# Optimization experiments

Hardware: AMD Instinct MI355X
Metric: run time of the kernel (lower is better)

Reference implementation:

```python
import jax, jax.numpy as jnp
import numpy as np

S, B, H = 2048, 4, 2048
NH = 16
HD = H // NH


def setup_inputs() -> dict:
    key = jax.random.key(0)
    ks = jax.random.split(key, 12)
    sc = 0.02
    return {
        "x": jax.random.normal(ks[0], (S, B, H), dtype=jnp.float32),
        "ln1_g": jnp.ones((H,), jnp.float32),
        "ln1_b": jnp.zeros((H,), jnp.float32),
        "qkv_w": jax.random.normal(ks[1], (3 * H, H), jnp.float32) * sc,
        "qkv_b": jnp.zeros((3 * H,), jnp.float32),
        "proj_w": jax.random.normal(ks[2], (H, H), jnp.float32) * sc,
        "proj_b": jnp.zeros((H,), jnp.float32),
        "ln2_g": jnp.ones((H,), jnp.float32),
        "ln2_b": jnp.zeros((H,), jnp.float32),
        "fc1_w": jax.random.normal(ks[3], (4 * H, H), jnp.float32) * sc,
        "fc1_b": jnp.zeros((4 * H,), jnp.float32),
        "fc2_w": jax.random.normal(ks[4], (H, 4 * H), jnp.float32) * sc,
        "fc2_b": jnp.zeros((H,), jnp.float32),
    }


def _layernorm(x, g, b, eps=1e-5):
    mu = jnp.mean(x, axis=-1, keepdims=True)
    var = jnp.mean((x - mu) ** 2, axis=-1, keepdims=True)
    return (x - mu) * jax.lax.rsqrt(var + eps) * g + b


def reference(x, ln1_g, ln1_b, qkv_w, qkv_b, proj_w, proj_b,
              ln2_g, ln2_b, fc1_w, fc1_b, fc2_w, fc2_b):
    # x: [S, B, H] (seq-first, as in original). Dropout is identity (eval mode).
    residual = x
    h = _layernorm(x, ln1_g, ln1_b)
    qkv = h @ qkv_w.T + qkv_b                       # [S, B, 3H]
    qkv = qkv.reshape(S, B, 3, NH, HD)
    q = jnp.transpose(qkv[:, :, 0], (1, 2, 0, 3))   # [B, NH, S, HD]
    k = jnp.transpose(qkv[:, :, 1], (1, 2, 0, 3))
    v = jnp.transpose(qkv[:, :, 2], (1, 2, 0, 3))
    scores = jnp.einsum("bhsd,bhtd->bhst", q, k) / jnp.sqrt(jnp.float32(HD))
    causal = jnp.tril(jnp.ones((S, S), dtype=bool))
    scores = jnp.where(causal, scores, jnp.float32(-jnp.inf))
    attn = jax.nn.softmax(scores, axis=-1)
    out = jnp.einsum("bhst,bhtd->bhsd", attn, v)    # [B, NH, S, HD]
    out = jnp.transpose(out, (2, 0, 1, 3)).reshape(S, B, H)
    out = out @ proj_w.T + proj_b
    x = residual + out
    residual = x
    h = _layernorm(x, ln2_g, ln2_b)
    h = h @ fc1_w.T + fc1_b
    h = jax.nn.gelu(h, approximate=False)
    h = h @ fc2_w.T + fc2_b
    return residual + h
```

## Files before the change

kernel.cpp:

```cpp
#include <hip/hip_runtime.h>
#include <hip/hip_bf16.h>
#include <cstdint>
#include <cstddef>

#define TOK 8192
#define HDIM 2048
#define H3 6144

typedef float f32x4 __attribute__((ext_vector_type(4)));
typedef short bf16x8 __attribute__((ext_vector_type(8)));
typedef int   i32x4 __attribute__((ext_vector_type(4)));
typedef unsigned short u16;
typedef unsigned int u32;
typedef u32 u32x2 __attribute__((ext_vector_type(2)));
typedef u32 u32x4 __attribute__((ext_vector_type(4)));

#define SLN  28.222222f
#define SW   1058.3333f
#define DQ   3.3480095e-5f

__device__ __forceinline__ u16 f2bf(float f) {
  union { float f; u32 u; } v; v.f = f;
  u32 u = v.u;
  return (u16)((u + 0x7fffu + ((u >> 16) & 1u)) >> 16);
}

__device__ __forceinline__ int q8(float v, float s) {
  int q = (int)rintf(v * s);
  return q < -127 ? -127 : (q > 127 ? 127 : q);
}

__device__ __forceinline__ float gelu_fast(float v) {
  const float u = 0.7978845608028654f * (v + 0.044715f * v * v * v);
  const float t = 1.0f - 2.0f / (__expf(2.0f * u) + 1.0f);
  return 0.5f * v * (1.0f + t);
}

__device__ __forceinline__ void gload16(const void* g, void* l) {
  __builtin_amdgcn_global_load_lds((const __attribute__((address_space(1))) u32*)g,
                                   (__attribute__((address_space(3))) u32*)l, 16, 0, 0);
}

#define GBAR()   __builtin_amdgcn_s_barrier()
#define GLGK0()  asm volatile("s_waitcnt lgkmcnt(0)" ::: "memory")
#define GVM(n)   asm volatile("s_waitcnt vmcnt(" #n ")" ::: "memory")
#define SCHED0() __builtin_amdgcn_sched_barrier(0)

__global__ __launch_bounds__(256)
void cvt_kernel(const float* __restrict__ in, u16* __restrict__ out, int n4) {
  int i = blockIdx.x * 256 + threadIdx.x;
  if (i >= n4) return;
  float4 v = ((const float4*)in)[i];
  union { u16 o[4]; u32x2 d; } t;
  t.o[0] = f2bf(v.x); t.o[1] = f2bf(v.y); t.o[2] = f2bf(v.z); t.o[3] = f2bf(v.w);
  ((u32x2*)out)[i] = t.d;
}

__global__ __launch_bounds__(256)
void cvt_i8_kernel(const float* __restrict__ in, char* __restrict__ out, int n4) {
  int i = blockIdx.x * 256 + threadIdx.x;
  if (i >= n4) return;
  float4 v = ((const float4*)in)[i];
  union { char c[4]; u32 d; } t;
  t.c[0] = (char)q8(v.x, SW); t.c[1] = (char)q8(v.y, SW);
  t.c[2] = (char)q8(v.z, SW); t.c[3] = (char)q8(v.w, SW);
  ((u32*)out)[i] = t.d;
}

template <int I8>
__global__ __launch_bounds__(256)
void ln_kernel(const float* __restrict__ x, const float* __restrict__ g,
               const float* __restrict__ bta, u16* __restrict__ out) {
  const int row = blockIdx.x, tid = threadIdx.x;
  const int lane = tid & 63, w = tid >> 6;
  const float* xr = x + (size_t)row * HDIM + tid * 8;
  float4 a = *(const float4*)xr;
  float4 c = *(const float4*)(xr + 4);
  float s = a.x + a.y + a.z + a.w + c.x + c.y + c.z + c.w;
  float q = a.x*a.x + a.y*a.y + a.z*a.z + a.w*a.w + c.x*c.x + c.y*c.y + c.z*c.z + c.w*c.w;
#pragma unroll
  for (int m = 32; m >= 1; m >>= 1) { s += __shfl_xor(s, m, 64); q += __shfl_xor(q, m, 64); }
  __shared__ float red[8];
  if (lane == 0) { red[w] = s; red[4 + w] = q; }
  __syncthreads();
  s = red[0] + red[1] + red[2] + red[3];
  q = red[4] + red[5] + red[6] + red[7];
  const float mu = s * (1.0f / HDIM);
  const float rstd = rsqrtf(q * (1.0f / HDIM) - mu * mu + 1e-5f);
  const float* gp = g + tid * 8; const float* bp = bta + tid * 8;
  float4 g0 = *(const float4*)gp, g1 = *(const float4*)(gp + 4);
  float4 b0 = *(const float4*)bp, b1 = *(const float4*)(bp + 4);
  float v[8];
  v[0] = (a.x - mu) * rstd * g0.x + b0.x;
  v[1] = (a.y - mu) * rstd * g0.y + b0.y;
  v[2] = (a.z - mu) * rstd * g0.z + b0.z;
  v[3] = (a.w - mu) * rstd * g0.w + b0.w;
  v[4] = (c.x - mu) * rstd * g1.x + b1.x;
  v[5] = (c.y - mu) * rstd * g1.y + b1.y;
  v[6] = (c.z - mu) * rstd * g1.z + b1.z;
  v[7] = (c.w - mu) * rstd * g1.w + b1.w;
  if constexpr (I8) {
    union { char c8[8]; u32x2 d; } t;
#pragma unroll
    for (int j = 0; j < 8; ++j) t.c8[j] = (char)q8(v[j], SLN);
    *(u32x2*)((char*)out + (size_t)row * HDIM + tid * 8) = t.d;
  } else {
    union { u16 o[8]; u32x4 d; } t;
#pragma unroll
    for (int j = 0; j < 8; ++j) t.o[j] = f2bf(v[j]);
    *(u32x4*)(out + (size_t)row * HDIM + tid * 8) = t.d;
  }
}

template <int EPI, int XSWZ>
__global__ __launch_bounds__(512, 1)
void gemm256(const u16* __restrict__ A, const u16* __restrict__ Bm,
             const float* __restrict__ bias, const float* __restrict__ resid,
             u16* __restrict__ Cb, float* __restrict__ Cf, int M, int N, int K) {
  __shared__ u16 lds[65536];
  char* Lb = (char*)lds;
  const int tid = threadIdx.x;
  const int lane = tid & 63, w = tid >> 6;
  const int wm = w >> 2, wn = w & 3;
  const int l15 = lane & 15, hi = lane >> 4;

  int tm, tn;
  if constexpr (XSWZ) {
    const int gx = gridDim.x;
    const int nwg = gx * gridDim.y;
    int wgid = blockIdx.y * gx + blockIdx.x;
    wgid = (wgid & 7) * (nwg >> 3) + (wgid >> 3);
    tm = (wgid / gx) * 256; tn = (wgid % gx) * 256;
  } else {
    tm = blockIdx.y * 256; tn = blockIdx.x * 256;
  }

  const size_t rsK = (size_t)K * 2;
  const int srow8 = tid >> 3;
  const int scb   = ((tid & 7) ^ ((tid >> 3) & 7)) * 16;
  const char* gA = (const char*)A + (size_t)(tm + srow8) * rsK + scb;
  const char* gB = (const char*)Bm + (size_t)(tn + srow8) * rsK + scb;

#define STGH(o, h, tt) do {                                                    \
    char* _d = Lb + ((((tt) & 1) << 16) + (o) * 32768 + (h) * 16384 + tid * 16); \
    const char* _s = (o) ? gB : gA;                                            \
    const size_t _off = (size_t)(tt) * 128 + (size_t)((h) * 128) * rsK;        \
    gload16(_s + _off, _d);                                                    \
    gload16(_s + _off + (size_t)64 * rsK, _d + 8192);                          \
  } while (0)

  int koff[2];
#pragma unroll
  for (int ks = 0; ks < 2; ++ks) koff[ks] = ((ks * 4 + hi) ^ (l15 & 7)) * 16;

#define LDA(qm, dst) do {                                                      \
    _Pragma("unroll")                                                          \
    for (int mi4 = 0; mi4 < 4; ++mi4)                                          \
      _Pragma("unroll")                                                        \
      for (int ks = 0; ks < 2; ++ks)                                           \
        dst[mi4][ks] = *(const bf16x8*)(Lb + bb + wm * 16384 +                 \
            ((qm) * 64 + mi4 * 16 + l15) * 128 + koff[ks]);                    \
  } while (0)

#define LDB(qn) do {                                                           \
    _Pragma("unroll")                                                          \
    for (int ni = 0; ni < 2; ++ni)                                             \
      _Pragma("unroll")                                                        \
      for (int ks = 0; ks < 2; ++ks)                                           \
        bf[ni][ks] = *(const bf16x8*)(Lb + bb + 32768 + (wn >> 1) * 16384 +    \
            ((wn & 1) * 64 + (qn) * 32 + ni * 16 + l15) * 128 + koff[ks]);     \
  } while (0)

#define MFMA16(qm, qn, src) do {                                               \
    __builtin_amdgcn_s_setprio(1);                                             \
    _Pragma("unroll")                                                          \
    for (int ks = 0; ks < 2; ++ks)                                             \
      _Pragma("unroll")                                                        \
      for (int mi4 = 0; mi4 < 4; ++mi4)                                        \
        _Pragma("unroll")                                                      \
        for (int ni = 0; ni < 2; ++ni)                                         \
          acc[(qm) * 4 + mi4][(qn) * 2 + ni] =                                 \
            __builtin_amdgcn_mfma_f32_16x16x32_bf16(src[mi4][ks], bf[ni][ks],  \
                acc[(qm) * 4 + mi4][(qn) * 2 + ni], 0, 0, 0);                  \
    __builtin_amdgcn_s_setprio(0);                                             \
  } while (0)

  f32x4 acc[8][4] = {};
  bf16x8 af0[4][2], af1[4][2], bf[2][2];

  const int NT = K >> 6;

  STGH(0, 0, 0); STGH(0, 1, 0); STGH(1, 0, 0); STGH(1, 1, 0);
  STGH(0, 0, 1); STGH(0, 1, 1);
  SCHED0(); GVM(4); GBAR();

  for (int t = 0; t < NT; ++t) {
    const int bb = (t & 1) << 16;
    const bool sB = (t + 1 < NT), sA = (t + 2 < NT);
    LDA(0, af0); LDB(0);
    if (sB) STGH(1, 0, t + 1);
    SCHED0(); GBAR(); GLGK0(); SCHED0(); MFMA16(0, 0, af0); GBAR();
    LDA(1, af1);
    if (sB) STGH(1, 1, t + 1);
    SCHED0(); GBAR(); GLGK0(); SCHED0(); MFMA16(1, 0, af1); GBAR();
    LDB(1);
    if (sA) STGH(0, 0, t + 2);
    SCHED0(); GBAR(); GLGK0(); SCHED0(); MFMA16(0, 1, af0); GBAR();
    if (sA) STGH(0, 1, t + 2);
    SCHED0(); MFMA16(1, 1, af1);
    if (sA) GVM(4); else GVM(0);
    GBAR();
  }

#pragma unroll
  for (int mi = 0; mi < 8; ++mi) {
#pragma unroll
    for (int ni = 0; ni < 4; ++ni) {
      const int col = tn + wn * 64 + ni * 16 + l15;
      const float bv = bias[col];
#pragma unroll
      for (int r = 0; r < 4; ++r) {
        const int row = tm + wm * 128 + mi * 16 + hi * 4 + r;
        float v = acc[mi][ni][r] + bv;
        if constexpr (EPI == 1) v = gelu_fast(v);
        const size_t idx = (size_t)row * N + col;
        if constexpr (EPI == 2) Cf[idx] = v + resid[idx];
        else                    Cb[idx] = f2bf(v);
      }
    }
  }
#undef STGH
#undef LDA
#undef LDB
#undef MFMA16
}

__global__ __launch_bounds__(512, 1)
void gemm256_i8(const char* __restrict__ A, const char* __restrict__ Bm,
                const float* __restrict__ bias, u16* __restrict__ Cb,
                int M, int N, int K) {
  __shared__ u16 lds[65536];
  char* Lb = (char*)lds;
  const int tid = threadIdx.x;
  const int lane = tid & 63, w = tid >> 6;
  const int wm = w >> 2, wn = w & 3;
  const int l15 = lane & 15, hi = lane >> 4;

  const int tm = blockIdx.y * 256, tn = blockIdx.x * 256;

  const size_t rsK = (size_t)K;
  const int srow8 = tid >> 3;
  const int scb   = ((tid & 7) ^ ((tid >> 3) & 7)) * 16;
  const char* gA = A + (size_t)(tm + srow8) * rsK + scb;
  const char* gB = Bm + (size_t)(tn + srow8) * rsK + scb;

#define STGH(o, h, tt) do {                                                    \
    char* _d = Lb + ((((tt) & 1) << 16) + (o) * 32768 + (h) * 16384 + tid * 16); \
    const char* _s = (o) ? gB : gA;                                            \
    const size_t _off = (size_t)(tt) * 128 + (size_t)((h) * 128) * rsK;        \
    gload16(_s + _off, _d);                                                    \
    gload16(_s + _off + (size_t)64 * rsK, _d + 8192);                          \
  } while (0)

  int koff[2];
#pragma unroll
  for (int ks = 0; ks < 2; ++ks) koff[ks] = ((ks * 4 + hi) ^ (l15 & 7)) * 16;

#define LDA(qm, dst) do {                                                      \
    _Pragma("unroll")                                                          \
    for (int mi4 = 0; mi4 < 4; ++mi4)                                          \
      _Pragma("unroll")                                                        \
      for (int ks = 0; ks < 2; ++ks)                                           \
        dst[mi4][ks] = *(const i32x4*)(Lb + bb + wm * 16384 +                  \
            ((qm) * 64 + mi4 * 16 + l15) * 128 + koff[ks]);                    \
  } while (0)

#define LDB(qn) do {                                                           \
    _Pragma("unroll")                                                          \
    for (int ni = 0; ni < 2; ++ni)                                             \
      _Pragma("unroll")                                                        \
      for (int ks = 0; ks < 2; ++ks)                                           \
        bfv[ni][ks] = *(const i32x4*)(Lb + bb + 32768 + (wn >> 1) * 16384 +    \
            ((wn & 1) * 64 + (qn) * 32 + ni * 16 + l15) * 128 + koff[ks]);     \
  } while (0)

#define MFMA16(qm, qn, src) do {                                               \
    __builtin_amdgcn_s_setprio(1);                                             \
    _Pragma("unroll")                                                          \
    for (int ks = 0; ks < 2; ++ks)                                             \
      _Pragma("unroll")                                                        \
      for (int mi4 = 0; mi4 < 4; ++mi4)                                        \
        _Pragma("unroll")                                                      \
        for (int ni = 0; ni < 2; ++ni)                                         \
          acc[(qm) * 4 + mi4][(qn) * 2 + ni] =                                 \
            __builtin_amdgcn_mfma_i32_16x16x64_i8(src[mi4][ks], bfv[ni][ks],   \
                acc[(qm) * 4 + mi4][(qn) * 2 + ni], 0, 0, 0);                  \
    __builtin_amdgcn_s_setprio(0);                                             \
  } while (0)

  i32x4 acc[8][4] = {};
  i32x4 af0[4][2], af1[4][2], bfv[2][2];

  const int NT = K >> 7;

  STGH(0, 0, 0); STGH(0, 1, 0); STGH(1, 0, 0); STGH(1, 1, 0);
  STGH(0, 0, 1); STGH(0, 1, 1);
  SCHED0(); GVM(4); GBAR();

  for (int t = 0; t < NT; ++t) {
    const int bb = (t & 1) << 16;
    const bool sB = (t + 1 < NT), sA = (t + 2 < NT);
    LDA(0, af0); LDB(0);
    if (sB) STGH(1, 0, t + 1);
    SCHED0(); GBAR(); GLGK0(); SCHED0(); MFMA16(0, 0, af0); GBAR();
    LDA(1, af1);
    if (sB) STGH(1, 1, t + 1);
    SCHED0(); GBAR(); GLGK0(); SCHED0(); MFMA16(1, 0, af1); GBAR();
    LDB(1);
    if (sA) STGH(0, 0, t + 2);
    SCHED0(); GBAR(); GLGK0(); SCHED0(); MFMA16(0, 1, af0); GBAR();
    if (sA) STGH(0, 1, t + 2);
    SCHED0(); MFMA16(1, 1, af1);
    if (sA) GVM(4); else GVM(0);
    GBAR();
  }

#pragma unroll
  for (int mi = 0; mi < 8; ++mi) {
#pragma unroll
    for (int ni = 0; ni < 4; ++ni) {
      const int col = tn + wn * 64 + ni * 16 + l15;
      const float bv = bias[col];
#pragma unroll
      for (int r = 0; r < 4; ++r) {
        const int row = tm + wm * 128 + mi * 16 + hi * 4 + r;
        float v = (float)acc[mi][ni][r] * DQ + bv;
        v = gelu_fast(v);
        Cb[(size_t)row * N + col] = f2bf(v);
      }
    }
  }
#undef STGH
#undef LDA
#undef LDB
#undef MFMA16
}

__global__ __launch_bounds__(256)
void vtrans_kernel(const u16* __restrict__ qkv, u16* __restrict__ vt) {
  __shared__ u16 tile[32 * 136];
  const int s0 = blockIdx.x * 32;
  const int bh = blockIdx.y;
  const int b = bh >> 4, h = bh & 15;
  const int t = threadIdx.x;
  const int srow = t >> 3, scol = (t & 7) * 16;
  const u16* src = qkv + (size_t)((s0 + srow) * 4 + b) * H3 + 4096 + h * 128 + scol;
  *(bf16x8*)(tile + srow * 136 + scol)     = *(const bf16x8*)src;
  *(bf16x8*)(tile + srow * 136 + scol + 8) = *(const bf16x8*)(src + 8);
  __syncthreads();
  const int d = t >> 1, sc = (t & 1) * 16;
  union { u16 o[16]; u32x4 q[2]; } tmp;
#pragma unroll
  for (int i = 0; i < 16; ++i) tmp.o[i] = tile[(sc + i) * 136 + d];
  u16* dst = vt + ((size_t)bh * 128 + d) * 2048 + s0 + sc;
  *(u32x4*)dst       = tmp.q[0];
  *(u32x4*)(dst + 8) = tmp.q[1];
}

__global__ __launch_bounds__(256, 2)
void attn_kernel(const u16* __restrict__ qkv, const u16* __restrict__ vt,
                 u16* __restrict__ outb) {
  const int qt = 15 - blockIdx.x;
  const int bh = blockIdx.y;
  const int b = bh >> 4, h = bh & 15;
  const int tid = threadIdx.x, lane = tid & 63, w = tid >> 6;
  const int hi = lane >> 4, l15 = lane & 15;
  const int qs = qt * 128;

  __shared__ u16 Klds[64 * 128];
  __shared__ u16 Vlds[128 * 64];
  __shared__ u16 Plds[4][2][1024];

  bf16x8 qf[2][4];
#pragma unroll
  for (int st = 0; st < 2; ++st) {
    const int qrow = qs + st * 64 + w * 16 + l15;
    const u16* qp = qkv + (size_t)(qrow * 4 + b) * H3 + h * 128 + hi * 8;
#pragma unroll
    for (int kc = 0; kc < 4; ++kc) qf[st][kc] = *(const bf16x8*)(qp + kc * 32);
  }

  f32x4 o0[8] = {}, o1[8] = {};
  float mr0 = -1e30f, lr0 = 0.0f, mr1 = -1e30f, lr1 = 0.0f;

  const float sc = 0.08838834764831845f;
  char* plb0 = (char*)&Plds[w][0][0];
  char* plb1 = (char*)&Plds[w][1][0];

  const int krow = tid >> 2;
  const int kcb  = (tid & 3) * 64;
  const int vd   = tid >> 1;
  const int vhb  = (tid & 1) * 64;

#define SMAX(sv, DOMASK, mrun, lrun, ov, plbx) do {                             \
    _Pragma("unroll")                                                           \
    for (int g = 0; g < 4; ++g)                                                 \
      _Pragma("unroll")                                                         \
      for (int r = 0; r < 4; ++r) sv[g][r] *= sc;                               \
    if (DOMASK) {                                                               \
      const int qrel = w * 16 + l15;                                            \
      _Pragma("unroll")                                                         \
      for (int g = 0; g < 4; ++g)                                               \
        _Pragma("unroll")                                                       \
        for (int r = 0; r < 4; ++r)                                             \
          if (g * 16 + hi * 4 + r > qrel) sv[g][r] = -1e30f;                    \
    }                                                                           \
    float pm = sv[0][0];                                                        \
    _Pragma("unroll")                                                           \
    for (int g = 0; g < 4; ++g)                                                 \
      _Pragma("unroll")                                                         \
      for (int r = 0; r < 4; ++r) pm = fmaxf(pm, sv[g][r]);                     \
    pm = fmaxf(pm, __shfl_xor(pm, 16, 64));                                     \
    pm = fmaxf(pm, __shfl_xor(pm, 32, 64));                                     \
    const float mnew = fmaxf(mrun, pm);                                         \
    const bool need = mnew > mrun;                                              \
    const float corr = __expf(mrun - mnew);                                     \
    mrun = mnew;                                                                \
    float p[4][4];                                                              \
    float rs = 0.0f;                                                            \
    _Pragma("unroll")                                                           \
    for (int g = 0; g < 4; ++g)                                                 \
      _Pragma("unroll")                                                         \
      for (int r = 0; r < 4; ++r) { p[g][r] = __expf(sv[g][r] - mnew); rs += p[g][r]; } \
    rs += __shfl_xor(rs, 16, 64);                                               \
    rs += __shfl_xor(rs, 32, 64);                                               \
    lrun = lrun * corr + rs;                                                    \
    if (__any(need)) {                                                          \
      float corrq[4];                                                           \
      _Pragma("unroll")                                                         \
      for (int r = 0; r < 4; ++r) corrq[r] = __shfl(corr, hi * 4 + r, 64);      \
      _Pragma("unroll")                                                         \
      for (int nf = 0; nf < 8; ++nf)                                            \
        _Pragma("unroll")                                                       \
        for (int r = 0; r < 4; ++r) ov[nf][r] *= corrq[r];                      \
    }                                                                           \
    _Pragma("unroll")                                                           \
    for (int g = 0; g < 4; ++g) {                                               \
      union { u16 h4[4]; u32x2 d; } pk;                                         \
      _Pragma("unroll")                                                         \
      for (int r = 0; r < 4; ++r) pk.h4[r] = f2bf(p[g][r]);                     \
      *(u32x2*)(plbx + ((l15 * 128 + g * 32 + hi * 8) ^ ((l15 & 7) << 4))) = pk.d; \
    }                                                                           \
  } while (0)

#define ATILE(DO0, M0, M1, kt_) do {                                            \
    const int kv0 = (kt_) * 64;                                                 \
    const u16* ksrc = qkv + (size_t)((kv0 + krow) * 4 + b) * H3 + 2048 + h * 128 + kcb / 2; \
    const u16* vsrc = vt + ((size_t)bh * 128 + vd) * 2048 + kv0 + (tid & 1) * 32; \
    bf16x8 kr[4], vr[4];                                                        \
    _Pragma("unroll")                                                           \
    for (int c = 0; c < 4; ++c) { kr[c] = *(const bf16x8*)(ksrc + c * 8);       \
                                  vr[c] = *(const bf16x8*)(vsrc + c * 8); }     \
    __syncthreads();                                                            \
    _Pragma("unroll")                                                           \
    for (int c = 0; c < 4; ++c) {                                               \
      *(bf16x8*)((char*)Klds + ((krow * 256 + kcb + c * 16) ^ ((krow & 7) << 4))) = kr[c]; \
      *(bf16x8*)((char*)Vlds + ((vd * 128 + vhb + c * 16) ^ ((vd & 7) << 4)))     = vr[c]; \
    }                                                                           \
    __syncthreads();                                                            \
    f32x4 s0[4] = {}, s1[4] = {};                                               \
    _Pragma("unroll")                                                           \
    for (int kc = 0; kc < 4; ++kc) {                                            \
      const int dbyte = kc * 64 + hi * 16;                                      \
      _Pragma("unroll")                                                         \
      for (int g = 0; g < 4; ++g) {                                             \
        const int row = g * 16 + l15;                                           \
        bf16x8 kf = *(const bf16x8*)((char*)Klds + ((row * 256 + dbyte) ^ ((l15 & 7) << 4))); \
        if (DO0) s0[g] = __builtin_amdgcn_mfma_f32_16x16x32_bf16(kf, qf[0][kc], s0[g], 0, 0, 0); \
        s1[g] = __builtin_amdgcn_mfma_f32_16x16x32_bf16(kf, qf[1][kc], s1[g], 0, 0, 0); \
      }                                                                         \
    }                                                                           \
    if (DO0) SMAX(s0, M0, mr0, lr0, o0, plb0);                                  \
    SMAX(s1, M1, mr1, lr1, o1, plb1);                                           \
    asm volatile("s_waitcnt lgkmcnt(0)" ::: "memory");                          \
    bf16x8 pf0[2], pf1[2];                                                      \
    _Pragma("unroll")                                                           \
    for (int hk = 0; hk < 2; ++hk) {                                            \
      const int po = (l15 * 128 + hk * 64 + hi * 16) ^ ((l15 & 7) << 4);        \
      if (DO0) pf0[hk] = *(const bf16x8*)(plb0 + po);                           \
      pf1[hk] = *(const bf16x8*)(plb1 + po);                                    \
    }                                                                           \
    _Pragma("unroll")                                                           \
    for (int hk = 0; hk < 2; ++hk)                                              \
      _Pragma("unroll")                                                         \
      for (int nf = 0; nf < 8; ++nf) {                                          \
        bf16x8 vf = *(const bf16x8*)((char*)Vlds +                              \
                      (((nf * 16 + l15) * 128 + hk * 64 + hi * 16) ^ ((l15 & 7) << 4))); \
        if (DO0) o0[nf] = __builtin_amdgcn_mfma_f32_16x16x32_bf16(pf0[hk], vf, o0[nf], 0, 0, 0); \
        o1[nf] = __builtin_amdgcn_mfma_f32_16x16x32_bf16(pf1[hk], vf, o1[nf], 0, 0, 0); \
      }                                                                         \
  } while (0)

  for (int kt = 0; kt <= 2 * qt; ++kt) {
    ATILE(1, (kt == 2 * qt), 0, kt);
  }
  {
    ATILE(0, 0, 1, 2 * qt + 1);
  }
#undef ATILE
#undef SMAX

#pragma unroll
  for (int st = 0; st < 2; ++st) {
    const float inv = 1.0f / (st ? lr1 : lr0);
    float invq[4];
#pragma unroll
    for (int r = 0; r < 4; ++r) invq[r] = __shfl(inv, hi * 4 + r, 64);
#pragma unroll
    for (int nf = 0; nf < 8; ++nf) {
#pragma unroll
      for (int r = 0; r < 4; ++r) {
        const int rl = hi * 4 + r;
        const int t = (qs + st * 64 + w * 16 + rl) * 4 + b;
        const f32x4* ov = st ? o1 : o0;
        outb[(size_t)t * HDIM + h * 128 + nf * 16 + l15] = f2bf(ov[nf][r] * invq[r]);
      }
    }
  }
}

extern "C" void kernel_launch(void* const* d_in, const int* in_sizes, int n_in,
                              void* d_out, int out_size, void* d_ws, size_t ws_size,
                              hipStream_t stream) {
  const float* x     = (const float*)d_in[0];
  const float* ln1g  = (const float*)d_in[1];
  const float* ln1b  = (const float*)d_in[2];
  const float* qkvw  = (const float*)d_in[3];
  const float* qkvb  = (const float*)d_in[4];
  const float* projw = (const float*)d_in[5];
  const float* projb = (const float*)d_in[6];
  const float* ln2g  = (const float*)d_in[7];
  const float* ln2b  = (const float*)d_in[8];
  const float* fc1w  = (const float*)d_in[9];
  const float* fc1b  = (const float*)d_in[10];
  const float* fc2w  = (const float*)d_in[11];
  const float* fc2b  = (const float*)d_in[12];
  float* out = (float*)d_out;

  u16* wbuf = (u16*)d_ws;
  u16* pbuf = (u16*)((char*)d_ws + (size_t)32 * 1024 * 1024);
  u16* qbuf = (u16*)((char*)d_ws + (size_t)64 * 1024 * 1024);
  u16* vtg  = (u16*)d_ws;
  u16* aout = (u16*)((char*)d_ws + (size_t)160 * 1024 * 1024);

  dim3 blk(256);
  dim3 gblk(512);

  ln_kernel<0><<<8192, blk, 0, stream>>>(x, ln1g, ln1b, pbuf);
  cvt_kernel<<<12288, blk, 0, stream>>>(qkvw, wbuf, 3145728);
  gemm256<0, 0><<<dim3(24, 32), gblk, 0, stream>>>(pbuf, wbuf, qkvb, nullptr, qbuf, nullptr, 8192, 6144, 2048);
  vtrans_kernel<<<dim3(64, 64), blk, 0, stream>>>(qbuf, vtg);
  attn_kernel<<<dim3(16, 64), blk, 0, stream>>>(qbuf, vtg, aout);
  cvt_kernel<<<4096, blk, 0, stream>>>(projw, wbuf, 1048576);
  gemm256<2, 0><<<dim3(8, 32), gblk, 0, stream>>>(aout, wbuf, projb, x, nullptr, out, 8192, 2048, 2048);
  ln_kernel<1><<<8192, blk, 0, stream>>>(out, ln2g, ln2b, pbuf);
  cvt_i8_kernel<<<16384, blk, 0, stream>>>(fc1w, (char*)wbuf, 4194304);
  gemm256_i8<<<dim3(32, 32), gblk, 0, stream>>>((const char*)pbuf, (const char*)wbuf, fc1b, qbuf, 8192, 8192, 2048);
  cvt_kernel<<<16384, blk, 0, stream>>>(fc2w, wbuf, 4194304);
  gemm256<2, 1><<<dim3(8, 32), gblk, 0, stream>>>(qbuf, wbuf, fc2b, out, nullptr, out, 8192, 2048, 8192);
}
```

Measured before the change: 962.9 us.

## Merge small prep kernels into combined launches and prefetch full next tile in GEMMs

Folds the layernorm, weight-conversion and V-transpose kernels into three combined launches that branch on block index, cutting launch count and letting independent prep work share the GPU. Workspace buffers are reassigned so the fused stages write to non-overlapping regions. The GEMM main loops now issue all four global-to-LDS stages for tile t+2 together instead of splitting B for t+1 and A for t+2, which changes the pipeline depth and vmcnt waits. That may change overlap and register or LDS pressure, and the buffer aliasing must stay correct.

```diff
diff --git a/kernel.cpp b/kernel.cpp
--- a/kernel.cpp
+++ b/kernel.cpp
@@ -46,20 +46,16 @@
 #define GVM(n)   asm volatile("s_waitcnt vmcnt(" #n ")" ::: "memory")
 #define SCHED0() __builtin_amdgcn_sched_barrier(0)
 
-__global__ __launch_bounds__(256)
-void cvt_kernel(const float* __restrict__ in, u16* __restrict__ out, int n4) {
-  int i = blockIdx.x * 256 + threadIdx.x;
-  if (i >= n4) return;
+__device__ __forceinline__ void cvt_body(const float* __restrict__ in,
+                                         u16* __restrict__ out, int i) {
   float4 v = ((const float4*)in)[i];
   union { u16 o[4]; u32x2 d; } t;
   t.o[0] = f2bf(v.x); t.o[1] = f2bf(v.y); t.o[2] = f2bf(v.z); t.o[3] = f2bf(v.w);
   ((u32x2*)out)[i] = t.d;
 }
 
-__global__ __launch_bounds__(256)
-void cvt_i8_kernel(const float* __restrict__ in, char* __restrict__ out, int n4) {
-  int i = blockIdx.x * 256 + threadIdx.x;
-  if (i >= n4) return;
+__device__ __forceinline__ void cvt_i8_body(const float* __restrict__ in,
+                                            char* __restrict__ out, int i) {
   float4 v = ((const float4*)in)[i];
   union { char c[4]; u32 d; } t;
   t.c[0] = (char)q8(v.x, SW); t.c[1] = (char)q8(v.y, SW);
@@ -68,10 +64,12 @@
 }
 
 template <int I8>
-__global__ __launch_bounds__(256)
-void ln_kernel(const float* __restrict__ x, const float* __restrict__ g,
-               const float* __restrict__ bta, u16* __restrict__ out) {
-  const int row = blockIdx.x, tid = threadIdx.x;
+__device__ __forceinline__ void ln_body(const float* __restrict__ x,
+                                        const float* __restrict__ g,
+                                        const float* __restrict__ bta,
+                                        u16* __restrict__ out, int row) {
+  __shared__ float red[8];
+  const int tid = threadIdx.x;
   const int lane = tid & 63, w = tid >> 6;
   const float* xr = x + (size_t)row * HDIM + tid * 8;
   float4 a = *(const float4*)xr;
@@ -80,7 +78,6 @@
   float q = a.x*a.x + a.y*a.y + a.z*a.z + a.w*a.w + c.x*c.x + c.y*c.y + c.z*c.z + c.w*c.w;
 #pragma unroll
   for (int m = 32; m >= 1; m >>= 1) { s += __shfl_xor(s, m, 64); q += __shfl_xor(q, m, 64); }
-  __shared__ float red[8];
   if (lane == 0) { red[w] = s; red[4 + w] = q; }
   __syncthreads();
   s = red[0] + red[1] + red[2] + red[3];
@@ -112,6 +109,55 @@
   }
 }
 
+__device__ __forceinline__ void vtrans_body(const u16* __restrict__ qkv,
+                                            u16* __restrict__ vt, int bid) {
+  __shared__ u16 tile[32 * 136];
+  const int s0 = (bid & 63) * 32;
+  const int bh = bid >> 6;
+  const int b = bh >> 4, h = bh & 15;
+  const int t = threadIdx.x;
+  const int srow = t >> 3, scol = (t & 7) * 16;
+  const u16* src = qkv + (size_t)((s0 + srow) * 4 + b) * H3 + 4096 + h * 128 + scol;
+  *(bf16x8*)(tile + srow * 136 + scol)     = *(const bf16x8*)src;
+  *(bf16x8*)(tile + srow * 136 + scol + 8) = *(const bf16x8*)(src + 8);
+  __syncthreads();
+  const int d = t >> 1, sc = (t & 1) * 16;
+  union { u16 o[16]; u32x4 q[2]; } tmp;
+#pragma unroll
+  for (int i = 0; i < 16; ++i) tmp.o[i] = tile[(sc + i) * 136 + d];
+  u16* dst = vt + ((size_t)bh * 128 + d) * 2048 + s0 + sc;
+  *(u32x4*)dst       = tmp.q[0];
+  *(u32x4*)(dst + 8) = tmp.q[1];
+}
+
+__global__ __launch_bounds__(256)
+void pre1_kernel(const float* __restrict__ x, const float* __restrict__ g,
+                 const float* __restrict__ bta, u16* __restrict__ lnout,
+                 const float* __restrict__ qw, u16* __restrict__ qwout) {
+  const int bid = blockIdx.x;
+  if (bid < 8192)  ln_body<0>(x, g, bta, lnout, bid);
+  else             cvt_body(qw, qwout, (bid - 8192) * 256 + threadIdx.x);
+}
+
+__global__ __launch_bounds__(256)
+void mid1_kernel(const u16* __restrict__ qkv, u16* __restrict__ vt,
+                 const float* __restrict__ pw, u16* __restrict__ pwout) {
+  const int bid = blockIdx.x;
+  if (bid < 4096)  vtrans_body(qkv, vt, bid);
+  else             cvt_body(pw, pwout, (bid - 4096) * 256 + threadIdx.x);
+}
+
+__global__ __launch_bounds__(256)
+void post1_kernel(const float* __restrict__ x2, const float* __restrict__ g,
+                  const float* __restrict__ bta, u16* __restrict__ lnout,
+                  const float* __restrict__ w1, char* __restrict__ w1out,
+                  const float* __restrict__ w2, u16* __restrict__ w2out) {
+  const int bid = blockIdx.x;
+  if (bid < 8192)       ln_body<1>(x2, g, bta, lnout, bid);
+  else if (bid < 24576) cvt_i8_body(w1, w1out, (bid - 8192) * 256 + threadIdx.x);
+  else                  cvt_body(w2, w2out, (bid - 24576) * 256 + threadIdx.x);
+}
+
 template <int EPI, int XSWZ>
 __global__ __launch_bounds__(512, 1)
 void gemm256(const u16* __restrict__ A, const u16* __restrict__ Bm,
@@ -191,24 +237,22 @@
   const int NT = K >> 6;
 
   STGH(0, 0, 0); STGH(0, 1, 0); STGH(1, 0, 0); STGH(1, 1, 0);
-  STGH(0, 0, 1); STGH(0, 1, 1);
-  SCHED0(); GVM(4); GBAR();
+  STGH(0, 0, 1); STGH(0, 1, 1); STGH(1, 0, 1); STGH(1, 1, 1);
+  SCHED0(); GVM(8); GBAR();
 
   for (int t = 0; t < NT; ++t) {
     const int bb = (t & 1) << 16;
-    const bool sB = (t + 1 < NT), sA = (t + 2 < NT);
+    const bool sN = (t + 2 < NT);
     LDA(0, af0); LDB(0);
-    if (sB) STGH(1, 0, t + 1);
     SCHED0(); GBAR(); GLGK0(); SCHED0(); MFMA16(0, 0, af0); GBAR();
     LDA(1, af1);
-    if (sB) STGH(1, 1, t + 1);
     SCHED0(); GBAR(); GLGK0(); SCHED0(); MFMA16(1, 0, af1); GBAR();
     LDB(1);
-    if (sA) STGH(0, 0, t + 2);
+    if (sN) STGH(0, 0, t + 2);
     SCHED0(); GBAR(); GLGK0(); SCHED0(); MFMA16(0, 1, af0); GBAR();
-    if (sA) STGH(0, 1, t + 2);
+    if (sN) { STGH(0, 1, t + 2); STGH(1, 0, t + 2); STGH(1, 1, t + 2); }
     SCHED0(); MFMA16(1, 1, af1);
-    if (sA) GVM(4); else GVM(0);
+    if (sN) GVM(8); else GVM(0);
     GBAR();
   }
 
@@ -304,24 +348,22 @@
   const int NT = K >> 7;
 
   STGH(0, 0, 0); STGH(0, 1, 0); STGH(1, 0, 0); STGH(1, 1, 0);
-  STGH(0, 0, 1); STGH(0, 1, 1);
-  SCHED0(); GVM(4); GBAR();
+  STGH(0, 0, 1); STGH(0, 1, 1); STGH(1, 0, 1); STGH(1, 1, 1);
+  SCHED0(); GVM(8); GBAR();
 
   for (int t = 0; t < NT; ++t) {
     const int bb = (t & 1) << 16;
-    const bool sB = (t + 1 < NT), sA = (t + 2 < NT);
+    const bool sN = (t + 2 < NT);
     LDA(0, af0); LDB(0);
-    if (sB) STGH(1, 0, t + 1);
     SCHED0(); GBAR(); GLGK0(); SCHED0(); MFMA16(0, 0, af0); GBAR();
     LDA(1, af1);
-    if (sB) STGH(1, 1, t + 1);
     SCHED0(); GBAR(); GLGK0(); SCHED0(); MFMA16(1, 0, af1); GBAR();
     LDB(1);
-    if (sA) STGH(0, 0, t + 2);
+    if (sN) STGH(0, 0, t + 2);
     SCHED0(); GBAR(); GLGK0(); SCHED0(); MFMA16(0, 1, af0); GBAR();
-    if (sA) STGH(0, 1, t + 2);
+    if (sN) { STGH(0, 1, t + 2); STGH(1, 0, t + 2); STGH(1, 1, t + 2); }
     SCHED0(); MFMA16(1, 1, af1);
-    if (sA) GVM(4); else GVM(0);
+    if (sN) GVM(8); else GVM(0);
     GBAR();
   }
 
@@ -344,27 +386,6 @@
 #undef LDA
 #undef LDB
 #undef MFMA16
-}
-
-__global__ __launch_bounds__(256)
-void vtrans_kernel(const u16* __restrict__ qkv, u16* __restrict__ vt) {
-  __shared__ u16 tile[32 * 136];
-  const int s0 = blockIdx.x * 32;
-  const int bh = blockIdx.y;
-  const int b = bh >> 4, h = bh & 15;
-  const int t = threadIdx.x;
-  const int srow = t >> 3, scol = (t & 7) * 16;
-  const u16* src = qkv + (size_t)((s0 + srow) * 4 + b) * H3 + 4096 + h * 128 + scol;
-  *(bf16x8*)(tile + srow * 136 + scol)     = *(const bf16x8*)src;
-  *(bf16x8*)(tile + srow * 136 + scol + 8) = *(const bf16x8*)(src + 8);
-  __syncthreads();
-  const int d = t >> 1, sc = (t & 1) * 16;
-  union { u16 o[16]; u32x4 q[2]; } tmp;
-#pragma unroll
-  for (int i = 0; i < 16; ++i) tmp.o[i] = tile[(sc + i) * 136 + d];
-  u16* dst = vt + ((size_t)bh * 128 + d) * 2048 + s0 + sc;
-  *(u32x4*)dst       = tmp.q[0];
-  *(u32x4*)(dst + 8) = tmp.q[1];
 }
 
 __global__ __launch_bounds__(256, 2)
@@ -547,25 +568,25 @@
   const float* fc2b  = (const float*)d_in[12];
   float* out = (float*)d_out;
 
-  u16* wbuf = (u16*)d_ws;
-  u16* pbuf = (u16*)((char*)d_ws + (size_t)32 * 1024 * 1024);
-  u16* qbuf = (u16*)((char*)d_ws + (size_t)64 * 1024 * 1024);
-  u16* vtg  = (u16*)d_ws;
-  u16* aout = (u16*)((char*)d_ws + (size_t)160 * 1024 * 1024);
+  u16*  wbuf  = (u16*)d_ws;
+  u16*  pbuf  = (u16*)((char*)d_ws + (size_t)32 * 1024 * 1024);
+  u16*  qbuf  = (u16*)((char*)d_ws + (size_t)64 * 1024 * 1024);
+  u16*  vtg   = (u16*)d_ws;
+  u16*  pw16  = (u16*)((char*)d_ws + (size_t)32 * 1024 * 1024);
+  u16*  fc2w16= (u16*)d_ws;
+  char* fc1i8 = (char*)d_ws + (size_t)32 * 1024 * 1024;
+  u16*  ln2i8 = (u16*)((char*)d_ws + (size_t)48 * 1024 * 1024);
+  u16*  aout  = (u16*)((char*)d_ws + (size_t)160 * 1024 * 1024);
 
   dim3 blk(256);
   dim3 gblk(512);
 
-  ln_kernel<0><<<8192, blk, 0, stream>>>(x, ln1g, ln1b, pbuf);
-  cvt_kernel<<<12288, blk, 0, stream>>>(qkvw, wbuf, 3145728);
+  pre1_kernel<<<20480, blk, 0, stream>>>(x, ln1g, ln1b, pbuf, qkvw, wbuf);
   gemm256<0, 0><<<dim3(24, 32), gblk, 0, stream>>>(pbuf, wbuf, qkvb, nullptr, qbuf, nullptr, 8192, 6144, 2048);
-  vtrans_kernel<<<dim3(64, 64), blk, 0, stream>>>(qbuf, vtg);
+  mid1_kernel<<<8192, blk, 0, stream>>>(qbuf, vtg, projw, pw16);
   attn_kernel<<<dim3(16, 64), blk, 0, stream>>>(qbuf, vtg, aout);
-  cvt_kernel<<<4096, blk, 0, stream>>>(projw, wbuf, 1048576);
-  gemm256<2, 0><<<dim3(8, 32), gblk, 0, stream>>>(aout, wbuf, projb, x, nullptr, out, 8192, 2048, 2048);
-  ln_kernel<1><<<8192, blk, 0, stream>>>(out, ln2g, ln2b, pbuf);
-  cvt_i8_kernel<<<16384, blk, 0, stream>>>(fc1w, (char*)wbuf, 4194304);
-  gemm256_i8<<<dim3(32, 32), gblk, 0, stream>>>((const char*)pbuf, (const char*)wbuf, fc1b, qbuf, 8192, 8192, 2048);
-  cvt_kernel<<<16384, blk, 0, stream>>>(fc2w, wbuf, 4194304);
-  gemm256<2, 1><<<dim3(8, 32), gblk, 0, stream>>>(qbuf, wbuf, fc2b, out, nullptr, out, 8192, 2048, 8192);
-}
+  gemm256<2, 0><<<dim3(8, 32), gblk, 0, stream>>>(aout, pw16, projb, x, nullptr, out, 8192, 2048, 2048);
+  post1_kernel<<<40960, blk, 0, stream>>>(out, ln2g, ln2b, ln2i8, fc1w, fc1i8, fc2w, fc2w16);
+  gemm256_i8<<<dim3(32, 32), gblk, 0, stream>>>((const char*)ln2i8, fc1i8, fc1b, qbuf, 8192, 8192, 2048);
+  gemm256<2, 1><<<dim3(8, 32), gblk, 0, stream>>>(qbuf, fc2w16, fc2b, out, nullptr, out, 8192, 2048, 8192);
+}
```

Measured after the change: 961.4 us. About the same (-0.2%).
